# Kernel optimization log

Measured on AMD Instinct MI355X. Metric: run time of the kernel, lower is better.

## Reference

```python
import math
import jax, jax.numpy as jnp
import numpy as np

B = 128          # batch_size (graphs)
SEQ = 128        # max_seq_len (nodes per graph)
D = 128          # input_dim
HID = 64         # enc_hidden_dim
HEADS = 4        # in_head
N = B * SEQ      # total nodes
E = 262144       # edges (avg degree 16)


def _make_pe(seq, d):
    pos = np.arange(seq, dtype=np.float32)[:, None]
    i_even = np.arange(0, d, 2, dtype=np.float32)
    pe = np.zeros((seq, d), dtype=np.float32)
    pe[:, 0::2] = np.sin(pos / 10000.0 ** (2.0 * i_even / d))
    pe[:, 1::2] = np.cos(pos / 10000.0 ** (2.0 * (i_even + 1.0) / d))
    return jnp.asarray(pe)


def setup_inputs() -> dict:
    key = jax.random.key(0)
    ks = jax.random.split(key, 10)
    s = 0.1
    return {
        "x": jax.random.normal(ks[0], (N, D), jnp.float32),
        "edge_index": jax.random.randint(ks[1], (2, E), 0, N),
        "pe": _make_pe(SEQ, D),
        "W1": jax.random.normal(ks[2], (D, HEADS * HID), jnp.float32) * s,
        "a_src1": jax.random.normal(ks[3], (HEADS, HID), jnp.float32) * s,
        "a_dst1": jax.random.normal(ks[4], (HEADS, HID), jnp.float32) * s,
        "b1": jnp.zeros((HEADS * HID,), jnp.float32),
        "W2": jax.random.normal(ks[5], (HEADS * HID, HID), jnp.float32) * s,
        "a_src2": jax.random.normal(ks[6], (1, HID), jnp.float32) * s,
        "a_dst2": jax.random.normal(ks[7], (1, HID), jnp.float32) * s,
        "b2": jnp.zeros((HID,), jnp.float32),
        "batch_size": B,
    }


def _gat_conv(x, src, dst, W, a_src, a_dst, b, heads, ch, concat, n):
    # PyG GATConv (eval mode, self-loops already appended to src/dst).
    h = (x @ W).reshape(n, heads, ch)                      # [N,H,C]
    alpha_src = jnp.einsum("nhc,hc->nh", h, a_src)         # [N,H]
    alpha_dst = jnp.einsum("nhc,hc->nh", h, a_dst)
    e = jax.nn.leaky_relu(alpha_src[src] + alpha_dst[dst], 0.2)  # [E,H]
    m = jax.ops.segment_max(e, dst, num_segments=n)        # segment softmax over dst
    ex = jnp.exp(e - m[dst])
    den = jax.ops.segment_sum(ex, dst, num_segments=n)
    alpha = ex / (den[dst] + 1e-16)                        # [E,H]
    out = jax.ops.segment_sum(h[src] * alpha[:, :, None], dst, num_segments=n)
    out = out.reshape(n, heads * ch) if concat else out.mean(axis=1)
    return out + b


def reference(x, edge_index, pe, W1, a_src1, a_dst1, b1, W2, a_src2, a_dst2, b2, batch_size):
    n = x.shape[0]
    loop = jnp.arange(n)
    src = jnp.concatenate([edge_index[0], loop])           # add self-loops (PyG default)
    dst = jnp.concatenate([edge_index[1], loop])
    # positional encoding (dropout inactive in eval)
    h = x * math.sqrt(x.shape[1]) + jnp.tile(pe, (batch_size, 1))
    h = jax.nn.elu(_gat_conv(h, src, dst, W1, a_src1, a_dst1, b1, HEADS, HID, True, n))
    out = _gat_conv(h, src, dst, W2, a_src2, a_dst2, b2, 1, HID, False, n)
    return out.reshape(batch_size, -1, out.shape[1])
```

## Files before the change

kernel.cpp:

```cpp
#include <hip/hip_runtime.h>
#include <hip/hip_bf16.h>

typedef __hip_bfloat16 bf16;
typedef __attribute__((ext_vector_type(8))) short short8v;
typedef __attribute__((ext_vector_type(4))) float f32x4;

#define N_NODES 16384
#define D_IN    128
#define HID     64
#define HEADS   4
#define F1      256
#define SEQ     128
#define SLOTS   64

__device__ __forceinline__ float wave_sum(float v) {
    #pragma unroll
    for (int o = 32; o > 0; o >>= 1) v += __shfl_xor(v, o, 64);
    return v;
}
__device__ __forceinline__ float lrelu(float v) { return v > 0.f ? v : 0.2f * v; }
__device__ __forceinline__ float bfu(unsigned short u) {
    return __uint_as_float((unsigned)u << 16);
}
__device__ __forceinline__ unsigned short f2b(float f) {
    unsigned u = __float_as_uint(f);
    return (unsigned short)((u + 0x7fffu + ((u >> 16) & 1u)) >> 16);
}

__global__ __launch_bounds__(256) void k_prep(const float* __restrict__ W1,
                                              const float* __restrict__ a_s1,
                                              const float* __restrict__ a_d1,
                                              unsigned short* __restrict__ w1hi,
                                              unsigned short* __restrict__ w1lo,
                                              float* __restrict__ gs,
                                              float* __restrict__ gd,
                                              int* __restrict__ cnt) {
    int gid = blockIdx.x * 256 + threadIdx.x;
    int j  = gid & 7;
    int l  = (gid >> 3) & 63;
    int ks = (gid >> 9) & 3;
    int n  = gid >> 11;
    int k   = ks * 32 + ((l >> 4) << 3) + j;
    int col = n * 16 + (l & 15);
    float w = W1[(size_t)k * 256 + col];
    unsigned short hi = f2b(w);
    w1hi[gid] = hi;
    w1lo[gid] = f2b(w - bfu(hi));
    if (gid < N_NODES) cnt[gid] = 0;
    if (gid < 512) {
        int kk = gid >> 2, hd = gid & 3;
        const float* wr = W1 + (size_t)kk * 256 + hd * 64;
        const float* as = a_s1 + hd * 64;
        const float* ad = a_d1 + hd * 64;
        float s = 0.f, d2 = 0.f;
        for (int c = 0; c < 64; c++) { float wv = wr[c]; s += wv * as[c]; d2 += wv * ad[c]; }
        gs[gid] = s; gd[gid] = d2;
    }
}

__global__ __launch_bounds__(256, 4) void k_gemm1m(const float* __restrict__ x,
                                                   const float* __restrict__ pe,
                                                   const unsigned short* __restrict__ w1hi,
                                                   const unsigned short* __restrict__ w1lo,
                                                   const float* __restrict__ gs,
                                                   const float* __restrict__ gd,
                                                   bf16* __restrict__ h,
                                                   float* __restrict__ as1,
                                                   float* __restrict__ ad1,
                                                   const int* __restrict__ ei, int E, int Etot,
                                                   int* __restrict__ cnt,
                                                   int* __restrict__ esrc) {
    int tid = threadIdx.x, lane = tid & 63, wv = tid >> 6;

    for (int e = blockIdx.x * 256 + tid; e < Etot; e += 131072) {
        int s, d;
        if (e < E) { s = ei[e]; d = ei[E + e]; }
        else       { s = e - E; d = s; }
        int pos = atomicAdd(&cnt[d], 1);
        if (pos < SLOTS) esrc[d * SLOTS + pos] = s;
    }

    int strip = blockIdx.x * 2 + (wv >> 1);
    int nhalf = wv & 1;
    int rowb = strip * 16;
    int r0 = lane & 15;
    int kg = lane >> 4;
    int kb = kg * 8;

    short8v afh[4], afl[4];
    f32x4 ls = {0.f, 0.f, 0.f, 0.f};
    f32x4 ld = {0.f, 0.f, 0.f, 0.f};
    #pragma unroll
    for (int ks = 0; ks < 4; ks++) {
        const float* xp = x  + (size_t)(rowb + r0) * 128 + ks * 32 + kb;
        const float* pp = pe + (size_t)((rowb + r0) & (SEQ - 1)) * 128 + ks * 32 + kb;
        float4 xa = *(const float4*)xp;
        float4 xb = *(const float4*)(xp + 4);
        float4 pa = *(const float4*)pp;
        float4 pb = *(const float4*)(pp + 4);
        float v[8];
        v[0] = xa.x * 11.313708499f + pa.x;
        v[1] = xa.y * 11.313708499f + pa.y;
        v[2] = xa.z * 11.313708499f + pa.z;
        v[3] = xa.w * 11.313708499f + pa.w;
        v[4] = xb.x * 11.313708499f + pb.x;
        v[5] = xb.y * 11.313708499f + pb.y;
        v[6] = xb.z * 11.313708499f + pb.z;
        v[7] = xb.w * 11.313708499f + pb.w;
        short8v ah, al;
        #pragma unroll
        for (int j = 0; j < 8; j++) {
            unsigned short hi = f2b(v[j]);
            ah[j] = (short)hi;
            al[j] = (short)f2b(v[j] - bfu(hi));
        }
        afh[ks] = ah; afl[ks] = al;
        if (nhalf == 0) {
            #pragma unroll
            for (int j = 0; j < 8; j++) {
                int k = ks * 32 + kb + j;
                float4 g4 = *(const float4*)(gs + k * 4);
                float4 h4 = *(const float4*)(gd + k * 4);
                ls.x += v[j] * g4.x; ls.y += v[j] * g4.y;
                ls.z += v[j] * g4.z; ls.w += v[j] * g4.w;
                ld.x += v[j] * h4.x; ld.y += v[j] * h4.y;
                ld.z += v[j] * h4.z; ld.w += v[j] * h4.w;
            }
        }
    }
    if (nhalf == 0) {
        #pragma unroll
        for (int o = 16; o < 64; o <<= 1) {
            ls.x += __shfl_xor(ls.x, o); ls.y += __shfl_xor(ls.y, o);
            ls.z += __shfl_xor(ls.z, o); ls.w += __shfl_xor(ls.w, o);
            ld.x += __shfl_xor(ld.x, o); ld.y += __shfl_xor(ld.y, o);
            ld.z += __shfl_xor(ld.z, o); ld.w += __shfl_xor(ld.w, o);
        }
        if (lane < 16) {
            int row = rowb + lane;
            *(float4*)(as1 + row * 4) = make_float4(ls.x, ls.y, ls.z, ls.w);
            *(float4*)(ad1 + row * 4) = make_float4(ld.x, ld.y, ld.z, ld.w);
        }
    }

    const short8v* wph = (const short8v*)w1hi;
    const short8v* wpl = (const short8v*)w1lo;
    unsigned short* hu = (unsigned short*)h;
    #pragma unroll
    for (int t = 0; t < 8; t++) {
        int n = nhalf * 8 + t;
        f32x4 acc = {0.f, 0.f, 0.f, 0.f};
        #pragma unroll
        for (int ks = 0; ks < 4; ks++) {
            short8v bh = wph[(n * 4 + ks) * 64 + lane];
            short8v bl = wpl[(n * 4 + ks) * 64 + lane];
            acc = __builtin_amdgcn_mfma_f32_16x16x32_bf16(afh[ks], bh, acc, 0, 0, 0);
            acc = __builtin_amdgcn_mfma_f32_16x16x32_bf16(afl[ks], bh, acc, 0, 0, 0);
            acc = __builtin_amdgcn_mfma_f32_16x16x32_bf16(afh[ks], bl, acc, 0, 0, 0);
        }
        #pragma unroll
        for (int r = 0; r < 4; r++)
            hu[(size_t)(rowb + kg * 4 + r) * 256 + n * 16 + r0] = f2b(acc[r]);
    }
}

__global__ __launch_bounds__(256) void k_agg1_gemm2(
        const int* __restrict__ cnt, const int* __restrict__ esrc,
        const float* __restrict__ as1, const float* __restrict__ ad1,
        const bf16* __restrict__ h,
        const float* __restrict__ b1,
        const float* __restrict__ W2,
        const float* __restrict__ a_src2, const float* __restrict__ a_dst2,
        bf16* __restrict__ h2, float* __restrict__ as2, float* __restrict__ ad2) {
    __shared__ float hs[4][256];
    __shared__ int2  sts[16][64];
    int tid = threadIdx.x, lane = tid & 63, wv = tid >> 6;
    int dbase = blockIdx.x * 4;

    int cv4 = cnt[dbase + (lane & 3)];

    #pragma unroll
    for (int it = 0; it < 4; it++) {
        int d = dbase + it;
        int deg = min(__shfl(cv4, it), SLOTS);
        int s = esrc[(size_t)d * SLOTS + lane] & (N_NODES - 1);
        float av = as1[(size_t)s * 4 + wv];
        float adw = ad1[d * 4 + wv];
        float t = (lane < deg) ? __expf(lrelu(av + adw) - 40.f) : 0.f;
        float inv = 1.f / wave_sum(t);
        int2 pr; pr.x = s; pr.y = __float_as_int(t * inv);
        sts[it * 4 + wv][lane] = pr;
    }

    const unsigned short* hb = (const unsigned short*)h + (size_t)wv * 64 + lane;
    float bb = b1[wv * 64 + lane];
    #pragma unroll 2
    for (int it = 0; it < 4; it++) {
        int deg = min(__shfl(cv4, it), SLOTS);
        const int4* row4 = (const int4*)sts[it * 4 + wv];
        int nq = (deg + 3) >> 2;
        float acc = 0.f;
        int4 A = row4[0];
        int4 B = row4[1];
        unsigned short e0 = hb[(size_t)A.x * 256];
        unsigned short e1 = hb[(size_t)A.z * 256];
        unsigned short e2 = hb[(size_t)B.x * 256];
        unsigned short e3 = hb[(size_t)B.z * 256];
        for (int q = 1; q < nq; q++) {
            int4 An = row4[2 * q];
            int4 Bn = row4[2 * q + 1];
            unsigned short f0 = hb[(size_t)An.x * 256];
            unsigned short f1 = hb[(size_t)An.z * 256];
            unsigned short f2 = hb[(size_t)Bn.x * 256];
            unsigned short f3 = hb[(size_t)Bn.z * 256];
            acc += bfu(e0) * __uint_as_float(A.y);
            acc += bfu(e1) * __uint_as_float(A.w);
            acc += bfu(e2) * __uint_as_float(B.y);
            acc += bfu(e3) * __uint_as_float(B.w);
            A = An; B = Bn; e0 = f0; e1 = f1; e2 = f2; e3 = f3;
        }
        acc += bfu(e0) * __uint_as_float(A.y);
        acc += bfu(e1) * __uint_as_float(A.w);
        acc += bfu(e2) * __uint_as_float(B.y);
        acc += bfu(e3) * __uint_as_float(B.w);
        float v = acc + bb;
        hs[it][wv * 64 + lane] = v > 0.f ? v : (__expf(v) - 1.f);
    }
    __syncthreads();

    float* part = (float*)sts;

    {
        float acc2[4] = {0, 0, 0, 0};
        const int k4base = wv * 16;
        for (int kk = 0; kk < 16; kk++) {
            int k4 = k4base + kk;
            const float* wp = W2 + (size_t)k4 * 256 + lane;
            float w0 = wp[0], w1 = wp[64], w2 = wp[128], w3 = wp[192];
            #pragma unroll
            for (int r = 0; r < 4; r++) {
                float4 u = *(const float4*)&hs[r][k4 * 4];
                acc2[r] += u.x * w0 + u.y * w1 + u.z * w2 + u.w * w3;
            }
        }
        #pragma unroll
        for (int r = 0; r < 4; r++) part[(wv * 4 + r) * 64 + lane] = acc2[r];
    }
    __syncthreads();
    {
        int r = wv;
        float a0 = part[(0 * 4 + r) * 64 + lane] + part[(1 * 4 + r) * 64 + lane]
                 + part[(2 * 4 + r) * 64 + lane] + part[(3 * 4 + r) * 64 + lane];
        float asj = a_src2[lane], adj = a_dst2[lane];
        int n0 = dbase + r;
        h2[(size_t)n0 * 64 + lane] = __float2bfloat16(a0);
        float va0 = wave_sum(a0 * asj);
        float vd0 = wave_sum(a0 * adj);
        if (lane == 0) {
            as2[n0] = va0; ad2[n0] = vd0;
        }
    }
}

__global__ __launch_bounds__(256) void k_agg2(const int* __restrict__ cnt,
                                              const int* __restrict__ esrc,
                                              const float* __restrict__ as2,
                                              const float* __restrict__ ad2,
                                              const bf16* __restrict__ h2,
                                              const float* __restrict__ b2v,
                                              float* __restrict__ out) {
    __shared__ int2 sts2[4][64];
    int tid = threadIdx.x, lane = tid & 63, wv = tid >> 6;
    int d = blockIdx.x * 4 + wv;
    int deg = min(cnt[d], SLOTS);

    int s = esrc[(size_t)d * SLOTS + lane] & (N_NODES - 1);
    float av = as2[s];
    float adw = ad2[d];
    float t = (lane < deg) ? __expf(lrelu(av + adw) - 40.f) : 0.f;
    float inv = 1.f / wave_sum(t);
    int2 pr; pr.x = s; pr.y = __float_as_int(t * inv);
    sts2[wv][lane] = pr;

    const unsigned short* hb = (const unsigned short*)h2 + lane;
    const int4* row4 = (const int4*)sts2[wv];
    int nq = (deg + 3) >> 2;
    float acc = 0.f;
    int4 A = row4[0];
    int4 B = row4[1];
    unsigned short e0 = hb[(size_t)A.x * 64];
    unsigned short e1 = hb[(size_t)A.z * 64];
    unsigned short e2 = hb[(size_t)B.x * 64];
    unsigned short e3 = hb[(size_t)B.z * 64];
    for (int q = 1; q < nq; q++) {
        int4 An = row4[2 * q];
        int4 Bn = row4[2 * q + 1];
        unsigned short f0 = hb[(size_t)An.x * 64];
        unsigned short f1 = hb[(size_t)An.z * 64];
        unsigned short f2 = hb[(size_t)Bn.x * 64];
        unsigned short f3 = hb[(size_t)Bn.z * 64];
        acc += bfu(e0) * __uint_as_float(A.y);
        acc += bfu(e1) * __uint_as_float(A.w);
        acc += bfu(e2) * __uint_as_float(B.y);
        acc += bfu(e3) * __uint_as_float(B.w);
        A = An; B = Bn; e0 = f0; e1 = f1; e2 = f2; e3 = f3;
    }
    acc += bfu(e0) * __uint_as_float(A.y);
    acc += bfu(e1) * __uint_as_float(A.w);
    acc += bfu(e2) * __uint_as_float(B.y);
    acc += bfu(e3) * __uint_as_float(B.w);
    out[(size_t)d * 64 + lane] = acc + b2v[lane];
}

extern "C" void kernel_launch(void* const* d_in, const int* in_sizes, int n_in,
                              void* d_out, int out_size, void* d_ws, size_t ws_size,
                              hipStream_t stream) {
    const float* x    = (const float*)d_in[0];
    const int*   ei   = (const int*)  d_in[1];
    const float* pe   = (const float*)d_in[2];
    const float* W1   = (const float*)d_in[3];
    const float* a_s1 = (const float*)d_in[4];
    const float* a_d1 = (const float*)d_in[5];
    const float* b1   = (const float*)d_in[6];
    const float* W2   = (const float*)d_in[7];
    const float* a_s2 = (const float*)d_in[8];
    const float* a_d2 = (const float*)d_in[9];
    const float* b2   = (const float*)d_in[10];

    const int E    = in_sizes[1] / 2;
    const int n    = N_NODES;
    const int Etot = E + n;

    char* p = (char*)d_ws;
    auto alloc = [&](size_t bytes) -> void* {
        void* r = (void*)p;
        p += (bytes + 255) & ~(size_t)255;
        return r;
    };
    int*   cnt     = (int*)  alloc((size_t)n * 4);
    int*   esrc    = (int*)  alloc((size_t)n * SLOTS * 4);
    bf16*  h       = (bf16*) alloc((size_t)n * F1 * 2);
    float* as1     = (float*)alloc((size_t)n * HEADS * 4);
    float* ad1     = (float*)alloc((size_t)n * HEADS * 4);
    bf16*  h2      = (bf16*) alloc((size_t)n * HID * 2);
    float* as2     = (float*)alloc((size_t)n * 4);
    float* ad2     = (float*)alloc((size_t)n * 4);
    unsigned short* w1hi = (unsigned short*)alloc((size_t)D_IN * F1 * 2);
    unsigned short* w1lo = (unsigned short*)alloc((size_t)D_IN * F1 * 2);
    float* gs      = (float*)alloc((size_t)D_IN * HEADS * 4);
    float* gd      = (float*)alloc((size_t)D_IN * HEADS * 4);

    k_prep      <<<128, 256, 0, stream>>>(W1, a_s1, a_d1, w1hi, w1lo, gs, gd, cnt);
    k_gemm1m    <<<n / 32, 256, 0, stream>>>(x, pe, w1hi, w1lo, gs, gd, h, as1, ad1,
                                             ei, E, Etot, cnt, esrc);
    k_agg1_gemm2<<<n / 4, 256, 0, stream>>>(cnt, esrc, as1, ad1, h, b1,
                                            W2, a_s2, a_d2, h2, as2, ad2);
    k_agg2      <<<n / 4, 256, 0, stream>>>(cnt, esrc, as2, ad2, h2, b2, (float*)d_out);
}
```

Before: 159.9 us.

## Assign one destination node per wave with vectorized 4-bf16 gathers in layer-1 aggregation

Layer-1 aggregation now maps each wave to one destination node instead of one head across four nodes. Each wave computes the attention softmax for all four heads at once using float4 loads of the per-node scores. It then gathers four bf16 features per lane with 8-byte loads rather than one 2-byte load per lane, cutting the number of memory instructions per edge and the index/weight LDS reads. Lanes are split into 16-lane groups per head, so each lane reads that head's weight. Each wave now carries its own node's degree, which can cause imbalance between waves in a block.

```diff
diff --git a/kernel.cpp b/kernel.cpp
--- a/kernel.cpp
+++ b/kernel.cpp
@@ -173,62 +173,76 @@
         const float* __restrict__ a_src2, const float* __restrict__ a_dst2,
         bf16* __restrict__ h2, float* __restrict__ as2, float* __restrict__ ad2) {
     __shared__ float hs[4][256];
-    __shared__ int2  sts[16][64];
+    __shared__ int2  st[4][4][64];
     int tid = threadIdx.x, lane = tid & 63, wv = tid >> 6;
     int dbase = blockIdx.x * 4;
-
-    int cv4 = cnt[dbase + (lane & 3)];
-
-    #pragma unroll
-    for (int it = 0; it < 4; it++) {
-        int d = dbase + it;
-        int deg = min(__shfl(cv4, it), SLOTS);
+    int d = dbase + wv;
+    int deg = min(cnt[d], SLOTS);
+
+    {
         int s = esrc[(size_t)d * SLOTS + lane] & (N_NODES - 1);
-        float av = as1[(size_t)s * 4 + wv];
-        float adw = ad1[d * 4 + wv];
-        float t = (lane < deg) ? __expf(lrelu(av + adw) - 40.f) : 0.f;
-        float inv = 1.f / wave_sum(t);
-        int2 pr; pr.x = s; pr.y = __float_as_int(t * inv);
-        sts[it * 4 + wv][lane] = pr;
-    }
-
-    const unsigned short* hb = (const unsigned short*)h + (size_t)wv * 64 + lane;
-    float bb = b1[wv * 64 + lane];
-    #pragma unroll 2
-    for (int it = 0; it < 4; it++) {
-        int deg = min(__shfl(cv4, it), SLOTS);
-        const int4* row4 = (const int4*)sts[it * 4 + wv];
-        int nq = (deg + 3) >> 2;
-        float acc = 0.f;
-        int4 A = row4[0];
-        int4 B = row4[1];
-        unsigned short e0 = hb[(size_t)A.x * 256];
-        unsigned short e1 = hb[(size_t)A.z * 256];
-        unsigned short e2 = hb[(size_t)B.x * 256];
-        unsigned short e3 = hb[(size_t)B.z * 256];
-        for (int q = 1; q < nq; q++) {
-            int4 An = row4[2 * q];
-            int4 Bn = row4[2 * q + 1];
-            unsigned short f0 = hb[(size_t)An.x * 256];
-            unsigned short f1 = hb[(size_t)An.z * 256];
-            unsigned short f2 = hb[(size_t)Bn.x * 256];
-            unsigned short f3 = hb[(size_t)Bn.z * 256];
-            acc += bfu(e0) * __uint_as_float(A.y);
-            acc += bfu(e1) * __uint_as_float(A.w);
-            acc += bfu(e2) * __uint_as_float(B.y);
-            acc += bfu(e3) * __uint_as_float(B.w);
-            A = An; B = Bn; e0 = f0; e1 = f1; e2 = f2; e3 = f3;
-        }
-        acc += bfu(e0) * __uint_as_float(A.y);
-        acc += bfu(e1) * __uint_as_float(A.w);
-        acc += bfu(e2) * __uint_as_float(B.y);
-        acc += bfu(e3) * __uint_as_float(B.w);
-        float v = acc + bb;
-        hs[it][wv * 64 + lane] = v > 0.f ? v : (__expf(v) - 1.f);
+        float4 av = *(const float4*)(as1 + (size_t)s * 4);
+        float4 dv = *(const float4*)(ad1 + (size_t)d * 4);
+        bool live = lane < deg;
+        float t0 = live ? __expf(lrelu(av.x + dv.x) - 40.f) : 0.f;
+        float t1 = live ? __expf(lrelu(av.y + dv.y) - 40.f) : 0.f;
+        float t2 = live ? __expf(lrelu(av.z + dv.z) - 40.f) : 0.f;
+        float t3 = live ? __expf(lrelu(av.w + dv.w) - 40.f) : 0.f;
+        float i0 = 1.f / wave_sum(t0);
+        float i1 = 1.f / wave_sum(t1);
+        float i2 = 1.f / wave_sum(t2);
+        float i3 = 1.f / wave_sum(t3);
+        int2 p0; p0.x = s; p0.y = __float_as_int(t0 * i0); st[wv][0][lane] = p0;
+        int2 p1; p1.x = s; p1.y = __float_as_int(t1 * i1); st[wv][1][lane] = p1;
+        int2 p2; p2.x = s; p2.y = __float_as_int(t2 * i2); st[wv][2][lane] = p2;
+        int2 p3; p3.x = s; p3.y = __float_as_int(t3 * i3); st[wv][3][lane] = p3;
+    }
+
+    {
+        int hd = lane >> 4;
+        const int4* stp4 = (const int4*)st[wv][hd];
+        const uint2* hb = (const uint2*)h;
+        float a0 = 0.f, a1 = 0.f, a2 = 0.f, a3 = 0.f;
+        int np = (deg + 1) >> 1;
+        int4 P = stp4[0];
+        uint2 u0 = hb[(size_t)P.x * 64 + lane];
+        uint2 u1 = hb[(size_t)P.z * 64 + lane];
+        for (int q = 1; q < np; q++) {
+            int4 Pn = stp4[q];
+            uint2 v0 = hb[(size_t)Pn.x * 64 + lane];
+            uint2 v1 = hb[(size_t)Pn.z * 64 + lane];
+            float ta = __uint_as_float(P.y), tb = __uint_as_float(P.w);
+            a0 += __uint_as_float(u0.x << 16) * ta;
+            a1 += __uint_as_float(u0.x & 0xffff0000u) * ta;
+            a2 += __uint_as_float(u0.y << 16) * ta;
+            a3 += __uint_as_float(u0.y & 0xffff0000u) * ta;
+            a0 += __uint_as_float(u1.x << 16) * tb;
+            a1 += __uint_as_float(u1.x & 0xffff0000u) * tb;
+            a2 += __uint_as_float(u1.y << 16) * tb;
+            a3 += __uint_as_float(u1.y & 0xffff0000u) * tb;
+            P = Pn; u0 = v0; u1 = v1;
+        }
+        float ta = __uint_as_float(P.y), tb = __uint_as_float(P.w);
+        a0 += __uint_as_float(u0.x << 16) * ta;
+        a1 += __uint_as_float(u0.x & 0xffff0000u) * ta;
+        a2 += __uint_as_float(u0.y << 16) * ta;
+        a3 += __uint_as_float(u0.y & 0xffff0000u) * ta;
+        a0 += __uint_as_float(u1.x << 16) * tb;
+        a1 += __uint_as_float(u1.x & 0xffff0000u) * tb;
+        a2 += __uint_as_float(u1.y << 16) * tb;
+        a3 += __uint_as_float(u1.y & 0xffff0000u) * tb;
+
+        float4 bb = *(const float4*)(b1 + lane * 4);
+        float o0 = a0 + bb.x, o1 = a1 + bb.y, o2 = a2 + bb.z, o3 = a3 + bb.w;
+        o0 = o0 > 0.f ? o0 : (__expf(o0) - 1.f);
+        o1 = o1 > 0.f ? o1 : (__expf(o1) - 1.f);
+        o2 = o2 > 0.f ? o2 : (__expf(o2) - 1.f);
+        o3 = o3 > 0.f ? o3 : (__expf(o3) - 1.f);
+        *(float4*)&hs[wv][lane * 4] = make_float4(o0, o1, o2, o3);
     }
     __syncthreads();
 
-    float* part = (float*)sts;
+    float* part = (float*)st;
 
     {
         float acc2[4] = {0, 0, 0, 0};
```

Result: faster. 155.2 us (-2.9%).
